# Performance work log

Measured on AMD Instinct MI355X. Metric: run time of the kernel, lower is better.

## Reference

```python
import jax, jax.numpy as jnp
import numpy as np

N = 100000      # nodes
E = 3200000     # edges (avg degree 32)
G = 64          # graphs in batch
IN_C = 128      # in_channels
HID = 16        # hidden_channels
OUT_C = 8       # out_channels
EDGE_C = 16     # edge_channels


def setup_inputs() -> dict:
    key = jax.random.key(0)
    ks = jax.random.split(key, 10)
    x = jax.random.normal(ks[0], (N, IN_C), dtype=jnp.float32)
    edge_index = jax.random.randint(ks[1], (2, E), 0, N, dtype=jnp.int64)
    edge_attr = jax.random.normal(ks[2], (E, EDGE_C), dtype=jnp.float32)
    batch_index = jnp.sort(jax.random.randint(ks[3], (N,), 0, G, dtype=jnp.int64))
    def lin(k, fan_in, fan_out):
        bound = 1.0 / np.sqrt(fan_in)
        return jax.random.uniform(k, (fan_in, fan_out), jnp.float32, -bound, bound)
    return {
        "x": x,
        "edge_index": edge_index,
        "edge_attr": edge_attr,
        "batch_index": batch_index,
        "W1_node": lin(ks[4], IN_C, HID),
        "W1_edge": lin(ks[5], EDGE_C, HID),
        "W2_node": lin(ks[6], HID, HID),
        "W2_edge": lin(ks[7], EDGE_C, HID),
        "node_W": lin(ks[8], HID, OUT_C),
        "node_b": jax.random.uniform(ks[9], (OUT_C,), jnp.float32, -1.0 / np.sqrt(HID), 1.0 / np.sqrt(HID)),
    }


def _gcn_conv(h, edge_attr_pad, src, dst, norm, W_node, W_edge, n_nodes):
    # node/edge linear transforms (no bias, as in lin_node/lin_edge)
    node_emb = h @ W_node                       # [N, H]
    edge_emb = edge_attr_pad @ W_edge           # [E+N, H]
    # message: norm * (x_j + edge_attr), scatter-add at destination
    msg = norm[:, None] * (node_emb[src] + edge_emb)
    return jax.ops.segment_sum(msg, dst, num_segments=n_nodes)


def reference(x, edge_index, edge_attr, batch_index,
              W1_node, W1_edge, W2_node, W2_edge, node_W, node_b):
    n = x.shape[0]
    loop = jnp.arange(n, dtype=edge_index.dtype)
    src = jnp.concatenate([edge_index[0], loop])          # add_self_loops
    dst = jnp.concatenate([edge_index[1], loop])
    ea = jnp.concatenate(
        [edge_attr, jnp.zeros((n, edge_attr.shape[1]), edge_attr.dtype)], axis=0)
    # symmetric gcn_norm: deg from target index, norm = d^-1/2[src]*d^-1/2[dst]
    deg = jax.ops.segment_sum(jnp.ones_like(src, dtype=x.dtype), dst, num_segments=n)
    dinv = jnp.where(deg > 0, jax.lax.rsqrt(jnp.maximum(deg, 1.0)), 0.0)
    norm = dinv[src] * dinv[dst]

    h = jax.nn.relu(_gcn_conv(x, ea, src, dst, norm, W1_node, W1_edge, n))
    h = jax.nn.relu(_gcn_conv(h, ea, src, dst, norm, W2_node, W2_edge, n))

    # global mean pool over graphs
    ones = jnp.ones((n,), x.dtype)
    counts = jax.ops.segment_sum(ones, batch_index, num_segments=G)
    pooled = jax.ops.segment_sum(h, batch_index, num_segments=G)
    pooled = pooled / jnp.maximum(counts, 1.0)[:, None]

    return pooled @ node_W + node_b
```

## Files before the change

### kernel.cpp

```cpp
#include <hip/hip_runtime.h>
#include <hip/hip_bf16.h>

#define IN_C   128
#define HID    16
#define OUT_C  8
#define EDGE_C 16
#define NG     64
#define NRANGE 8
#define BSHIFT 7
#define BNODES 128
#define LCAP   5120

__global__ void deg_kernel(const int* __restrict__ dst, int* __restrict__ deg, int E) {
    int e = blockIdx.x * blockDim.x + threadIdx.x;
    if (e < E) atomicAdd(&deg[dst[e]], 1);
}

__global__ void scanA_kernel(const int* __restrict__ deg, int* __restrict__ row_start,
                             int* __restrict__ blocksum, int n) {
    __shared__ int s[256];
    int t = threadIdx.x;
    int i = blockIdx.x * 256 + t;
    int own = (i < n) ? deg[i] : 0;
    s[t] = own; __syncthreads();
    for (int off = 1; off < 256; off <<= 1) {
        int v = (t >= off) ? s[t - off] : 0;
        __syncthreads();
        s[t] += v;
        __syncthreads();
    }
    if (i < n) row_start[i] = s[t] - own;
    if (t == 255) blocksum[blockIdx.x] = s[255];
}

__global__ void scanB_kernel(int* __restrict__ blocksum, int nb) {
    __shared__ int s[512];
    int t = threadIdx.x;
    int own = (t < nb) ? blocksum[t] : 0;
    s[t] = own; __syncthreads();
    for (int off = 1; off < 512; off <<= 1) {
        int v = (t >= off) ? s[t - off] : 0;
        __syncthreads();
        s[t] += v;
        __syncthreads();
    }
    if (t < nb) blocksum[t] = s[t] - own;
}

__global__ void scanC_kernel(const int* __restrict__ deg, int* __restrict__ row_start,
                             const int* __restrict__ blocksum,
                             float* __restrict__ dinv, int n) {
    int i = blockIdx.x * 256 + threadIdx.x;
    if (i < n) {
        row_start[i] = row_start[i] + blocksum[blockIdx.x];
        dinv[i] = rsqrtf((float)deg[i] + 1.0f);
    }
}

__global__ void bin_kernel(const int* __restrict__ src, const int* __restrict__ dst,
                           const int* __restrict__ row_start, int* __restrict__ bcur,
                           int2* __restrict__ adj, int E, int range_size, int bpr) {
    int r = blockIdx.x & (NRANGE - 1);
    int q = blockIdx.x >> 3;
    int lo = r * range_size;
    int hi = lo + range_size;
    long long chunk = ((long long)E + bpr - 1) / bpr;
    int e0 = (int)((long long)q * chunk);
    long long e1l = (long long)e0 + chunk;
    int e1 = (e1l < E) ? (int)e1l : E;
#pragma unroll 4
    for (int e = e0 + threadIdx.x; e < e1; e += blockDim.x) {
        int d = __builtin_nontemporal_load(dst + e);
        if (d >= lo && d < hi) {
            int s = __builtin_nontemporal_load(src + e);
            int b = d >> BSHIFT;
            int base = row_start[d & ~(BNODES - 1)];
            int pos = base + atomicAdd(&bcur[b << 4], 1);
            adj[pos] = make_int2(e, s | ((d & (BNODES - 1)) << 25));
        }
    }
}

__global__ void csr_kernel(int2* __restrict__ adj, const int* __restrict__ row_start,
                           int n, int E) {
    __shared__ int2 buf[LCAP];
    __shared__ int  rs[BNODES + 1];
    __shared__ int  cnt[BNODES];
    int b = blockIdx.x;
    int lo = b << BSHIFT;
    int t = threadIdx.x;
    for (int i = t; i < BNODES + 1; i += 256) {
        int node = lo + i;
        rs[i] = (node < n) ? row_start[node] : E;
    }
    for (int i = t; i < BNODES; i += 256) cnt[i] = 0;
    __syncthreads();
    int base = rs[0];
    int span = lo + BNODES;
    int end  = (span <= n) ? rs[BNODES] : rs[n - lo];
    int L = end - base;
    if (L > LCAP) L = LCAP;
    for (int i = t; i < L; i += 256) buf[i] = adj[base + i];
    __syncthreads();
    for (int i = t; i < L; i += 256) {
        int2 v = buf[i];
        int dl = ((unsigned)v.y) >> 25;
        int s  = v.y & ((1 << 25) - 1);
        int pos = rs[dl] + atomicAdd(&cnt[dl], 1);
        adj[pos] = make_int2(v.x, s);
    }
}

__global__ void xform1_kernel(const float* __restrict__ x, const float* __restrict__ W,
                              const float* __restrict__ dinv, float* __restrict__ a1, int n) {
    int t = threadIdx.x;
    int v = blockIdx.x * 16 + (t >> 4);
    int c = t & 15;
    if (v >= n) return;
    const float4* xr = (const float4*)(x + (size_t)v * IN_C);
    float acc = 0.0f;
#pragma unroll
    for (int k4 = 0; k4 < IN_C / 4; ++k4) {
        float4 xv = xr[k4];
        int k = k4 * 4;
        acc += xv.x * W[(k + 0) * HID + c];
        acc += xv.y * W[(k + 1) * HID + c];
        acc += xv.z * W[(k + 2) * HID + c];
        acc += xv.w * W[(k + 3) * HID + c];
    }
    a1[(size_t)v * HID + c] = dinv[v] * acc;
}

__global__ void gather1_kernel(const int2* __restrict__ adj, const int* __restrict__ row_start,
                               const int* __restrict__ deg,
                               const float* __restrict__ edge_attr,
                               const float* __restrict__ W1e, const float* __restrict__ W2n,
                               const float* __restrict__ a1, const float* __restrict__ dinv,
                               float* __restrict__ a2, float* __restrict__ ES, int n) {
    int t = threadIdx.x;
    int lane = t & 63;
    int slot = lane >> 4;
    int c = lane & 15;
    float we[EDGE_C], wn[HID];
#pragma unroll
    for (int k = 0; k < EDGE_C; ++k) we[k] = W1e[k * HID + c];
#pragma unroll
    for (int k = 0; k < HID; ++k) wn[k] = W2n[k * HID + c];
    int v = blockIdx.x * 4 + (t >> 6);
    if (v >= n) return;
    int start = row_start[v];
    int dg = deg[v];
    float es = 0.0f, s1 = 0.0f;
    for (int base = 0; base < dg; base += 64) {
        int m = dg - base; if (m > 64) m = 64;
        int e_my = 0, s_my = 0;
        float ds_my = 0.0f;
        if (lane < m) {
            long long adv = __builtin_nontemporal_load(
                (const long long*)&adj[start + base + lane]);
            e_my = (int)(adv & 0xffffffffLL);
            s_my = (int)(adv >> 32);
            ds_my = dinv[s_my];
        }
#pragma unroll 4
        for (int i = slot; i < m; i += 4) {
            int e = __shfl(e_my, i, 64);
            int s = __shfl(s_my, i, 64);
            float ds = __shfl(ds_my, i, 64);
            es += ds * __builtin_nontemporal_load(edge_attr + (size_t)e * EDGE_C + c);
            s1 += a1[s * HID + c];
        }
    }
    es += __shfl_xor(es, 16, 64); es += __shfl_xor(es, 32, 64);
    s1 += __shfl_xor(s1, 16, 64); s1 += __shfl_xor(s1, 32, 64);
    float dv = dinv[v];
    int lanebase = lane & ~15;
    float e1 = 0.0f;
#pragma unroll
    for (int k = 0; k < EDGE_C; ++k)
        e1 += __shfl(es, lanebase + k, 64) * we[k];
    float h = fmaxf(dv * (s1 + a1[(size_t)v * HID + c] + e1), 0.0f);
    float o = 0.0f;
#pragma unroll
    for (int k = 0; k < HID; ++k)
        o += __shfl(h, lanebase + k, 64) * wn[k];
    if (slot == 0) {
        a2[(size_t)v * HID + c] = dv * o;
        ES[(size_t)v * HID + c] = es;
    }
}

__global__ void gather2_kernel(const int2* __restrict__ adj, const int* __restrict__ row_start,
                               const int* __restrict__ deg,
                               const float* __restrict__ W2e,
                               const float* __restrict__ a2, const float* __restrict__ dinv,
                               const float* __restrict__ ES, float* __restrict__ h2, int n) {
    int t = threadIdx.x;
    int lane = t & 63;
    int slot = lane >> 4;
    int c = lane & 15;
    float we[EDGE_C];
#pragma unroll
    for (int k = 0; k < EDGE_C; ++k) we[k] = W2e[k * HID + c];
    int v = blockIdx.x * 4 + (t >> 6);
    if (v >= n) return;
    int start = row_start[v];
    int dg = deg[v];
    float s2 = 0.0f;
    for (int base = 0; base < dg; base += 64) {
        int m = dg - base; if (m > 64) m = 64;
        int s_my = 0;
        if (lane < m) {
            long long adv = __builtin_nontemporal_load(
                (const long long*)&adj[start + base + lane]);
            s_my = (int)(adv >> 32);
        }
#pragma unroll 4
        for (int i = slot; i < m; i += 4) {
            int s = __shfl(s_my, i, 64);
            s2 += a2[s * HID + c];
        }
    }
    s2 += __shfl_xor(s2, 16, 64); s2 += __shfl_xor(s2, 32, 64);
    float dv = dinv[v];
    int lanebase = lane & ~15;
    float esv = ES[(size_t)v * HID + c];
    float e2 = 0.0f;
#pragma unroll
    for (int k = 0; k < EDGE_C; ++k)
        e2 += __shfl(esv, lanebase + k, 64) * we[k];
    float h = fmaxf(dv * (s2 + a2[(size_t)v * HID + c] + e2), 0.0f);
    if (slot == 0) h2[(size_t)v * HID + c] = h;
}

__global__ void pool_final_kernel(const float* __restrict__ h2,
                                  const int* __restrict__ batch,
                                  const float* __restrict__ W, const float* __restrict__ b,
                                  float* __restrict__ out, int n) {
    __shared__ float sdata[256];
    int g = blockIdx.x;
    int t = threadIdx.x;
    int c = t & 15;
    int lo = 0, hi = n;
    while (lo < hi) { int m = (lo + hi) >> 1; if (batch[m] < g) lo = m + 1; else hi = m; }
    int start = lo;
    hi = n;
    while (lo < hi) { int m = (lo + hi) >> 1; if (batch[m] < g + 1) lo = m + 1; else hi = m; }
    int end = lo;
    float acc = 0.0f;
    for (int v = start + (t >> 4); v < end; v += 16)
        acc += h2[(size_t)v * HID + c];
    sdata[t] = acc; __syncthreads();
    for (int s = 128; s >= 16; s >>= 1) {
        if (t < s) sdata[t] += sdata[t + s];
        __syncthreads();
    }
    if (t < OUT_C) {
        float inv = 1.0f / fmaxf((float)(end - start), 1.0f);
        float o = b[t];
#pragma unroll
        for (int cc = 0; cc < HID; ++cc)
            o += sdata[cc] * inv * W[cc * OUT_C + t];
        out[g * OUT_C + t] = o;
    }
}

extern "C" void kernel_launch(void* const* d_in, const int* in_sizes, int n_in,
                              void* d_out, int out_size, void* d_ws, size_t ws_size,
                              hipStream_t stream) {
    const float* x         = (const float*)d_in[0];
    const int*   edge_idx  = (const int*)d_in[1];
    const float* edge_attr = (const float*)d_in[2];
    const int*   batch     = (const int*)d_in[3];
    const float* W1_node   = (const float*)d_in[4];
    const float* W1_edge   = (const float*)d_in[5];
    const float* W2_node   = (const float*)d_in[6];
    const float* W2_edge   = (const float*)d_in[7];
    const float* node_W    = (const float*)d_in[8];
    const float* node_b    = (const float*)d_in[9];
    float* out = (float*)d_out;

    const int N = in_sizes[0] / IN_C;
    const int E = in_sizes[1] / 2;
    const int* src = edge_idx;
    const int* dst = edge_idx + E;

    char* p = (char*)d_ws;
    int2*  adj       = (int2*)p;   p += sizeof(int2) * (size_t)E;
    int*   deg       = (int*)p;    p += sizeof(int) * (size_t)N;
    int*   bcur      = (int*)p;    p += sizeof(int) * 16384;
    int*   row_start = (int*)p;    p += sizeof(int) * (size_t)N;
    int*   blocksum  = (int*)p;    p += sizeof(int) * 512;
    float* dinv      = (float*)p;  p += sizeof(float) * (size_t)N;
    float* a1        = (float*)p;  p += sizeof(float) * (size_t)HID * N;
    float* a2        = (float*)p;  p += sizeof(float) * (size_t)HID * N;
    float* ES        = (float*)p;  p += sizeof(float) * (size_t)HID * N;
    float* h2        = a1;

    hipMemsetAsync(deg, 0, sizeof(int) * ((size_t)N + 16384), stream);

    const int tb = 256;
    const int nbN = (N + 255) / 256;
    deg_kernel <<<(E + tb - 1) / tb, tb, 0, stream>>>(dst, deg, E);
    scanA_kernel<<<nbN, 256, 0, stream>>>(deg, row_start, blocksum, N);
    scanB_kernel<<<1, 512, 0, stream>>>(blocksum, nbN);
    scanC_kernel<<<nbN, 256, 0, stream>>>(deg, row_start, blocksum, dinv, N);

    const int range_size = (N + NRANGE - 1) / NRANGE;
    const int bpr = 256;
    bin_kernel<<<NRANGE * bpr, tb, 0, stream>>>(src, dst, row_start, bcur, adj, E, range_size, bpr);
    const int nbuck = (N + BNODES - 1) >> BSHIFT;
    csr_kernel<<<nbuck, 256, 0, stream>>>(adj, row_start, N, E);

    xform1_kernel<<<(N + 15) / 16, tb, 0, stream>>>(x, W1_node, dinv, a1, N);

    gather1_kernel<<<(N + 3) / 4, tb, 0, stream>>>(
        adj, row_start, deg, edge_attr, W1_edge, W2_node, a1, dinv, a2, ES, N);
    gather2_kernel<<<(N + 3) / 4, tb, 0, stream>>>(
        adj, row_start, deg, W2_edge, a2, dinv, ES, h2, N);

    pool_final_kernel<<<NG, 256, 0, stream>>>(h2, batch, node_W, node_b, out, N);
}
```

Measured before the change: 935.5 us.

## Drop CSR sort pass; aggregate per 32-node bucket with shared-memory atomics

Removes the csr_kernel that sorted edges within each bucket. Buckets shrink to 32 nodes, and the two gather kernels now walk each bucket's unsorted edge list with one block per bucket. They accumulate into per-node shared-memory arrays with atomicAdd, then apply the small dense transforms out of shared memory. This saves a full read and write pass over the adjacency array, at the cost of shared-memory atomic contention and more buckets in bin_kernel's atomic counters.

```diff
diff --git a/kernel.cpp b/kernel.cpp
--- a/kernel.cpp
+++ b/kernel.cpp
@@ -7,9 +7,9 @@
 #define EDGE_C 16
 #define NG     64
 #define NRANGE 8
-#define BSHIFT 7
-#define BNODES 128
-#define LCAP   5120
+#define BSHIFT 5
+#define BNODES 32
+#define NBUCK_MAX 4096
 
 __global__ void deg_kernel(const int* __restrict__ dst, int* __restrict__ deg, int E) {
     int e = blockIdx.x * blockDim.x + threadIdx.x;
@@ -81,36 +81,6 @@
     }
 }
 
-__global__ void csr_kernel(int2* __restrict__ adj, const int* __restrict__ row_start,
-                           int n, int E) {
-    __shared__ int2 buf[LCAP];
-    __shared__ int  rs[BNODES + 1];
-    __shared__ int  cnt[BNODES];
-    int b = blockIdx.x;
-    int lo = b << BSHIFT;
-    int t = threadIdx.x;
-    for (int i = t; i < BNODES + 1; i += 256) {
-        int node = lo + i;
-        rs[i] = (node < n) ? row_start[node] : E;
-    }
-    for (int i = t; i < BNODES; i += 256) cnt[i] = 0;
-    __syncthreads();
-    int base = rs[0];
-    int span = lo + BNODES;
-    int end  = (span <= n) ? rs[BNODES] : rs[n - lo];
-    int L = end - base;
-    if (L > LCAP) L = LCAP;
-    for (int i = t; i < L; i += 256) buf[i] = adj[base + i];
-    __syncthreads();
-    for (int i = t; i < L; i += 256) {
-        int2 v = buf[i];
-        int dl = ((unsigned)v.y) >> 25;
-        int s  = v.y & ((1 << 25) - 1);
-        int pos = rs[dl] + atomicAdd(&cnt[dl], 1);
-        adj[pos] = make_int2(v.x, s);
-    }
-}
-
 __global__ void xform1_kernel(const float* __restrict__ x, const float* __restrict__ W,
                               const float* __restrict__ dinv, float* __restrict__ a1, int n) {
     int t = threadIdx.x;
@@ -131,106 +101,124 @@
     a1[(size_t)v * HID + c] = dinv[v] * acc;
 }
 
-__global__ void gather1_kernel(const int2* __restrict__ adj, const int* __restrict__ row_start,
-                               const int* __restrict__ deg,
+__global__ void gatherA_kernel(const int2* __restrict__ adj, const int* __restrict__ row_start,
                                const float* __restrict__ edge_attr,
                                const float* __restrict__ W1e, const float* __restrict__ W2n,
                                const float* __restrict__ a1, const float* __restrict__ dinv,
-                               float* __restrict__ a2, float* __restrict__ ES, int n) {
-    int t = threadIdx.x;
-    int lane = t & 63;
-    int slot = lane >> 4;
-    int c = lane & 15;
-    float we[EDGE_C], wn[HID];
-#pragma unroll
-    for (int k = 0; k < EDGE_C; ++k) we[k] = W1e[k * HID + c];
-#pragma unroll
-    for (int k = 0; k < HID; ++k) wn[k] = W2n[k * HID + c];
-    int v = blockIdx.x * 4 + (t >> 6);
-    if (v >= n) return;
-    int start = row_start[v];
-    int dg = deg[v];
-    float es = 0.0f, s1 = 0.0f;
-    for (int base = 0; base < dg; base += 64) {
-        int m = dg - base; if (m > 64) m = 64;
-        int e_my = 0, s_my = 0;
-        float ds_my = 0.0f;
-        if (lane < m) {
-            long long adv = __builtin_nontemporal_load(
-                (const long long*)&adj[start + base + lane]);
-            e_my = (int)(adv & 0xffffffffLL);
-            s_my = (int)(adv >> 32);
-            ds_my = dinv[s_my];
+                               float* __restrict__ a2, float* __restrict__ ES_g,
+                               int n, int E) {
+    __shared__ float S1[BNODES * HID];
+    __shared__ float ESs[BNODES * HID];
+    __shared__ float Hs[BNODES * HID];
+    __shared__ float W1s[EDGE_C * HID];
+    __shared__ float W2s[HID * HID];
+    int t = threadIdx.x;
+    int b = blockIdx.x;
+    int lo = b << BSHIFT;
+    W1s[t] = W1e[t];
+    W2s[t] = W2n[t];
+    S1[t] = 0.0f; S1[t + 256] = 0.0f;
+    ESs[t] = 0.0f; ESs[t + 256] = 0.0f;
+    __syncthreads();
+    int base = row_start[lo];
+    int hi_node = lo + BNODES;
+    int end = (hi_node < n) ? row_start[hi_node] : E;
+    int slot = t >> 4;
+    int c = t & 15;
+#pragma unroll 4
+    for (int i = base + slot; i < end; i += 16) {
+        long long adv = __builtin_nontemporal_load((const long long*)&adj[i]);
+        int e = (int)(adv & 0xffffffffLL);
+        int y = (int)(adv >> 32);
+        int s  = y & ((1 << 25) - 1);
+        int dl = ((unsigned)y) >> 25;
+        float ds = dinv[s];
+        float ea = __builtin_nontemporal_load(edge_attr + (size_t)e * EDGE_C + c);
+        float av = a1[s * HID + c];
+        atomicAdd(&ESs[dl * HID + c], ds * ea);
+        atomicAdd(&S1[dl * HID + c], av);
+    }
+    __syncthreads();
+#pragma unroll
+    for (int half = 0; half < 2; ++half) {
+        int nl = half * 16 + slot;
+        int v = lo + nl;
+        float h = 0.0f;
+        if (v < n) {
+            float dv = dinv[v];
+            float e1 = 0.0f;
+#pragma unroll
+            for (int k = 0; k < EDGE_C; ++k)
+                e1 += ESs[nl * HID + k] * W1s[k * HID + c];
+            h = fmaxf(dv * (S1[nl * HID + c] + a1[(size_t)v * HID + c] + e1), 0.0f);
         }
-#pragma unroll 4
-        for (int i = slot; i < m; i += 4) {
-            int e = __shfl(e_my, i, 64);
-            int s = __shfl(s_my, i, 64);
-            float ds = __shfl(ds_my, i, 64);
-            es += ds * __builtin_nontemporal_load(edge_attr + (size_t)e * EDGE_C + c);
-            s1 += a1[s * HID + c];
+        Hs[nl * HID + c] = h;
+    }
+    __syncthreads();
+#pragma unroll
+    for (int half = 0; half < 2; ++half) {
+        int nl = half * 16 + slot;
+        int v = lo + nl;
+        if (v < n) {
+            float o = 0.0f;
+#pragma unroll
+            for (int k = 0; k < HID; ++k)
+                o += Hs[nl * HID + k] * W2s[k * HID + c];
+            a2[(size_t)v * HID + c] = dinv[v] * o;
+            ES_g[(size_t)v * HID + c] = ESs[nl * HID + c];
         }
     }
-    es += __shfl_xor(es, 16, 64); es += __shfl_xor(es, 32, 64);
-    s1 += __shfl_xor(s1, 16, 64); s1 += __shfl_xor(s1, 32, 64);
-    float dv = dinv[v];
-    int lanebase = lane & ~15;
-    float e1 = 0.0f;
-#pragma unroll
-    for (int k = 0; k < EDGE_C; ++k)
-        e1 += __shfl(es, lanebase + k, 64) * we[k];
-    float h = fmaxf(dv * (s1 + a1[(size_t)v * HID + c] + e1), 0.0f);
-    float o = 0.0f;
-#pragma unroll
-    for (int k = 0; k < HID; ++k)
-        o += __shfl(h, lanebase + k, 64) * wn[k];
-    if (slot == 0) {
-        a2[(size_t)v * HID + c] = dv * o;
-        ES[(size_t)v * HID + c] = es;
-    }
-}
-
-__global__ void gather2_kernel(const int2* __restrict__ adj, const int* __restrict__ row_start,
-                               const int* __restrict__ deg,
+}
+
+__global__ void gatherB_kernel(const int2* __restrict__ adj, const int* __restrict__ row_start,
                                const float* __restrict__ W2e,
                                const float* __restrict__ a2, const float* __restrict__ dinv,
-                               const float* __restrict__ ES, float* __restrict__ h2, int n) {
-    int t = threadIdx.x;
-    int lane = t & 63;
-    int slot = lane >> 4;
-    int c = lane & 15;
-    float we[EDGE_C];
-#pragma unroll
-    for (int k = 0; k < EDGE_C; ++k) we[k] = W2e[k * HID + c];
-    int v = blockIdx.x * 4 + (t >> 6);
-    if (v >= n) return;
-    int start = row_start[v];
-    int dg = deg[v];
-    float s2 = 0.0f;
-    for (int base = 0; base < dg; base += 64) {
-        int m = dg - base; if (m > 64) m = 64;
-        int s_my = 0;
-        if (lane < m) {
-            long long adv = __builtin_nontemporal_load(
-                (const long long*)&adj[start + base + lane]);
-            s_my = (int)(adv >> 32);
+                               const float* __restrict__ ES_g, float* __restrict__ h2,
+                               int n, int E) {
+    __shared__ float S2[BNODES * HID];
+    __shared__ float ESs[BNODES * HID];
+    __shared__ float Ws[EDGE_C * HID];
+    int t = threadIdx.x;
+    int b = blockIdx.x;
+    int lo = b << BSHIFT;
+    Ws[t] = W2e[t];
+    S2[t] = 0.0f; S2[t + 256] = 0.0f;
+    {
+        size_t nb16 = (size_t)n * HID;
+        size_t i0 = (size_t)lo * HID + t;
+        ESs[t]       = (i0 < nb16)       ? ES_g[i0]       : 0.0f;
+        ESs[t + 256] = (i0 + 256 < nb16) ? ES_g[i0 + 256] : 0.0f;
+    }
+    __syncthreads();
+    int base = row_start[lo];
+    int hi_node = lo + BNODES;
+    int end = (hi_node < n) ? row_start[hi_node] : E;
+    int slot = t >> 4;
+    int c = t & 15;
+#pragma unroll 4
+    for (int i = base + slot; i < end; i += 16) {
+        long long adv = __builtin_nontemporal_load((const long long*)&adj[i]);
+        int y = (int)(adv >> 32);
+        int s  = y & ((1 << 25) - 1);
+        int dl = ((unsigned)y) >> 25;
+        float av = a2[s * HID + c];
+        atomicAdd(&S2[dl * HID + c], av);
+    }
+    __syncthreads();
+#pragma unroll
+    for (int half = 0; half < 2; ++half) {
+        int nl = half * 16 + slot;
+        int v = lo + nl;
+        if (v < n) {
+            float dv = dinv[v];
+            float e2 = 0.0f;
+#pragma unroll
+            for (int k = 0; k < EDGE_C; ++k)
+                e2 += ESs[nl * HID + k] * Ws[k * HID + c];
+            float h = fmaxf(dv * (S2[nl * HID + c] + a2[(size_t)v * HID + c] + e2), 0.0f);
+            h2[(size_t)v * HID + c] = h;
         }
-#pragma unroll 4
-        for (int i = slot; i < m; i += 4) {
-            int s = __shfl(s_my, i, 64);
-            s2 += a2[s * HID + c];
-        }
-    }
-    s2 += __shfl_xor(s2, 16, 64); s2 += __shfl_xor(s2, 32, 64);
-    float dv = dinv[v];
-    int lanebase = lane & ~15;
-    float esv = ES[(size_t)v * HID + c];
-    float e2 = 0.0f;
-#pragma unroll
-    for (int k = 0; k < EDGE_C; ++k)
-        e2 += __shfl(esv, lanebase + k, 64) * we[k];
-    float h = fmaxf(dv * (s2 + a2[(size_t)v * HID + c] + e2), 0.0f);
-    if (slot == 0) h2[(size_t)v * HID + c] = h;
+    }
 }
 
 __global__ void pool_final_kernel(const float* __restrict__ h2,
@@ -288,7 +276,7 @@
     char* p = (char*)d_ws;
     int2*  adj       = (int2*)p;   p += sizeof(int2) * (size_t)E;
     int*   deg       = (int*)p;    p += sizeof(int) * (size_t)N;
-    int*   bcur      = (int*)p;    p += sizeof(int) * 16384;
+    int*   bcur      = (int*)p;    p += sizeof(int) * NBUCK_MAX * 16;
     int*   row_start = (int*)p;    p += sizeof(int) * (size_t)N;
     int*   blocksum  = (int*)p;    p += sizeof(int) * 512;
     float* dinv      = (float*)p;  p += sizeof(float) * (size_t)N;
@@ -297,7 +285,7 @@
     float* ES        = (float*)p;  p += sizeof(float) * (size_t)HID * N;
     float* h2        = a1;
 
-    hipMemsetAsync(deg, 0, sizeof(int) * ((size_t)N + 16384), stream);
+    hipMemsetAsync(deg, 0, sizeof(int) * ((size_t)N + NBUCK_MAX * 16), stream);
 
     const int tb = 256;
     const int nbN = (N + 255) / 256;
@@ -309,15 +297,14 @@
     const int range_size = (N + NRANGE - 1) / NRANGE;
     const int bpr = 256;
     bin_kernel<<<NRANGE * bpr, tb, 0, stream>>>(src, dst, row_start, bcur, adj, E, range_size, bpr);
+
+    xform1_kernel<<<(N + 15) / 16, tb, 0, stream>>>(x, W1_node, dinv, a1, N);
+
     const int nbuck = (N + BNODES - 1) >> BSHIFT;
-    csr_kernel<<<nbuck, 256, 0, stream>>>(adj, row_start, N, E);
-
-    xform1_kernel<<<(N + 15) / 16, tb, 0, stream>>>(x, W1_node, dinv, a1, N);
-
-    gather1_kernel<<<(N + 3) / 4, tb, 0, stream>>>(
-        adj, row_start, deg, edge_attr, W1_edge, W2_node, a1, dinv, a2, ES, N);
-    gather2_kernel<<<(N + 3) / 4, tb, 0, stream>>>(
-        adj, row_start, deg, W2_edge, a2, dinv, ES, h2, N);
+    gatherA_kernel<<<nbuck, 256, 0, stream>>>(
+        adj, row_start, edge_attr, W1_edge, W2_node, a1, dinv, a2, ES, N, E);
+    gatherB_kernel<<<nbuck, 256, 0, stream>>>(
+        adj, row_start, W2_edge, a2, dinv, ES, h2, N, E);
 
     pool_final_kernel<<<NG, 256, 0, stream>>>(h2, batch, node_W, node_b, out, N);
 }
```

Measured after the change: 1.495 ms. 1.6x slower.
